# Optimization experiments

Hardware: AMD Instinct MI355X
Metric: run time of the kernel (lower is better)

The kernel has to match this reference:

```python
import jax, jax.numpy as jnp
import numpy as np

N = 50000      # nodes
E = 800000     # edges (avg degree 16)
IN, HID, OUT = 96, 96, 32


def _glorot(key, fan_in, fan_out):
    s = jnp.sqrt(2.0 / (fan_in + fan_out)).astype(jnp.float32)
    return jax.random.normal(key, (fan_in, fan_out), dtype=jnp.float32) * s


def setup_inputs() -> dict:
    key = jax.random.key(0)
    k = jax.random.split(key, 6)
    x = jax.random.normal(k[0], (N, IN), dtype=jnp.float32)
    edge_index = jax.random.randint(k[1], (2, E), 0, N)
    W1 = _glorot(k[2], IN, HID)
    b1 = jnp.zeros((HID,), dtype=jnp.float32)
    W2 = _glorot(k[3], HID, OUT)
    b2 = jnp.zeros((OUT,), dtype=jnp.float32)
    return {"x": x, "edge_index": edge_index, "W1": W1, "b1": b1, "W2": W2, "b2": b2}


def _add_self_loops(edge_index, n):
    loop = jnp.arange(n, dtype=edge_index.dtype)
    src = jnp.concatenate([edge_index[0], loop])
    dst = jnp.concatenate([edge_index[1], loop])
    return src, dst


def _gcn_conv(x, src, dst, W, b, n):
    # PyG GCNConv: linear transform, symmetric deg^-1/2 normalization, scatter-add, bias.
    h = x @ W                                            # [N, F_out]
    ones = jnp.ones(src.shape[0], dtype=x.dtype)
    deg = jax.ops.segment_sum(ones, dst, num_segments=n)  # in-degree incl. self loop
    dinv = jnp.where(deg > 0, jax.lax.rsqrt(deg), 0.0)
    norm = dinv[src] * dinv[dst]                         # [E+N]
    msg = h[src] * norm[:, None]                         # gather + scale
    out = jax.ops.segment_sum(msg, dst, num_segments=n)  # scatter-add
    return out + b


def reference(x, edge_index, W1, b1, W2, b2):
    n = x.shape[0]
    src, dst = _add_self_loops(edge_index, n)
    x1 = jax.nn.relu(_gcn_conv(x, src, dst, W1, b1, n))
    # dropout(p=0.5) is identity in eval mode
    out = _gcn_conv(x1, src, dst, W2, b2, n)
    return (x1, out)
```

## Files before the change

kernel.cpp:

```cpp
#include <hip/hip_runtime.h>


#define NBINS_CAP 256
#define MAXBLK 512
#define CHUNK 2048
#define EBUF 6144
#define WT_LD 104

typedef short short8 __attribute__((ext_vector_type(8)));
typedef float f32x4 __attribute__((ext_vector_type(4)));

__device__ __forceinline__ unsigned short f2bf(float f) {
    unsigned u = __float_as_uint(f);
    u = u + 0x7FFFu + ((u >> 16) & 1u);
    return (unsigned short)(u >> 16);
}
__device__ __forceinline__ float bflo(unsigned w) { return __uint_as_float(w << 16); }
__device__ __forceinline__ float bfhi(unsigned w) { return __uint_as_float(w & 0xFFFF0000u); }

template <int NT>
__global__ __launch_bounds__(NT) void binA_kernel(const int* __restrict__ src,
                                                  const int* __restrict__ dst,
                                                  unsigned* __restrict__ slab,
                                                  int* __restrict__ cntT,
                                                  int* __restrict__ segT,
                                                  int nbins, int E) {
    constexpr int PT = CHUNK / NT;
    __shared__ unsigned ebuf[CHUNK];
    __shared__ int hist[NBINS_CAP];
    __shared__ int cur[NBINS_CAP];
    __shared__ int sc[NT];
    const int tid = threadIdx.x;
    const int beg = blockIdx.x * CHUNK;
    const int cntE = min(CHUNK, E - beg);
    for (int i = tid; i < nbins; i += NT) hist[i] = 0;
    __syncthreads();
    unsigned pv[PT];
    int pb[PT];
#pragma unroll
    for (int j = 0; j < PT; ++j) {
        int idx = j * NT + tid;
        if (idx < cntE) {
            int e = beg + idx;
            int s = src[e], d = dst[e];
            pb[j] = d >> 8;
            pv[j] = ((unsigned)(d & 255) << 16) | (unsigned)s;
            atomicAdd(&hist[pb[j]], 1);
        } else {
            pb[j] = -1;
        }
    }
    __syncthreads();
    int v = (tid < nbins) ? hist[tid] : 0;
    sc[tid] = v;
    __syncthreads();
    for (int off = 1; off < NT; off <<= 1) {
        int t = (tid >= off) ? sc[tid - off] : 0;
        __syncthreads();
        sc[tid] += t;
        __syncthreads();
    }
    if (tid < nbins) cur[tid] = sc[tid] - v;
    __syncthreads();
#pragma unroll
    for (int j = 0; j < PT; ++j) {
        if (pb[j] >= 0) {
            int pos = atomicAdd(&cur[pb[j]], 1);
            ebuf[pos] = pv[j];
        }
    }
    __syncthreads();
    for (int i = tid; i < cntE; i += NT) slab[beg + i] = ebuf[i];
    for (int i = tid; i < nbins; i += NT) {
        cntT[i * MAXBLK + blockIdx.x] = hist[i];
        segT[i * MAXBLK + blockIdx.x] = cur[i] - hist[i];
    }
}

__global__ __launch_bounds__(256) void binsum_kernel(const int* __restrict__ cntT,
                                                     int* __restrict__ btotal,
                                                     const float* __restrict__ W1,
                                                     const float* __restrict__ W2,
                                                     unsigned short* __restrict__ wtg,
                                                     unsigned short* __restrict__ wtg2,
                                                     int nbins, int nblk) {
    __shared__ int r[256];
    const int bin = blockIdx.x, tid = threadIdx.x;
    int s = 0;
    for (int b = tid; b < nblk; b += 256) s += cntT[bin * MAXBLK + b];
    r[tid] = s;
    __syncthreads();
    for (int off = 128; off; off >>= 1) {
        if (tid < off) r[tid] += r[tid + off];
        __syncthreads();
    }
    if (tid == 0) btotal[bin] = r[0];
    const int total = 96 * 96 + 96 * 32;
    const int per = (total + nbins - 1) / nbins;
    for (int j = tid; j < per; j += 256) {
        int idx = bin * per + j;
        if (idx < 96 * 96) {
            int k = idx / 96, f = idx % 96;
            wtg[f * WT_LD + k] = f2bf(W1[idx]);
        } else if (idx < total) {
            int i2 = idx - 96 * 96;
            int k = i2 / 32, f = i2 % 32;
            wtg2[f * WT_LD + k] = f2bf(W2[i2]);
        }
    }
}

__global__ __launch_bounds__(512) void binB_kernel(const unsigned* __restrict__ slab,
                                                   const int* __restrict__ cntT,
                                                   const int* __restrict__ segT,
                                                   const int* __restrict__ btotal,
                                                   float* __restrict__ dinv,
                                                   int* __restrict__ row_ptr,
                                                   unsigned short* __restrict__ esrc,
                                                   int n, int nbins, int nblk, int E) {
    constexpr int NT = 512;
    __shared__ int segc[MAXBLK], pref[MAXBLK], sgs[MAXBLK];
    __shared__ unsigned ebuf[EBUF];
    __shared__ int sc[NT];
    __shared__ int bsc[256];
    __shared__ int hist[256], lbase[256], cur[256];
    const int tid = threadIdx.x;
    const int bin = blockIdx.x;

    if (tid < 256) bsc[tid] = (tid < nbins) ? btotal[tid] : 0;
    __syncthreads();
    for (int off = 1; off < 256; off <<= 1) {
        int t = 0;
        if (tid < 256 && tid >= off) t = bsc[tid - off];
        __syncthreads();
        if (tid < 256) bsc[tid] += t;
        __syncthreads();
    }
    const int base = (bin > 0) ? bsc[bin - 1] : 0;
    if (bin == nbins - 1 && tid == 0) row_ptr[n] = E;
    __syncthreads();

    for (int b = tid; b < MAXBLK; b += NT) {
        segc[b] = (b < nblk) ? cntT[bin * MAXBLK + b] : 0;
        sgs[b]  = (b < nblk) ? segT[bin * MAXBLK + b] : 0;
    }
    if (tid < 256) hist[tid] = 0;
    __syncthreads();
    int v = segc[tid];
    sc[tid] = v;
    __syncthreads();
    for (int off = 1; off < NT; off <<= 1) {
        int t = (tid >= off) ? sc[tid - off] : 0;
        __syncthreads();
        sc[tid] += t;
        __syncthreads();
    }
    pref[tid] = sc[tid] - v;
    __syncthreads();
    const int total = sc[NT - 1];
    const bool fits = (total <= EBUF);

    if (fits) {
        if (tid < nblk) {
            int c = segc[tid];
            const unsigned* p = slab + (size_t)tid * CHUNK + sgs[tid];
            int o = pref[tid];
            for (int i = 0; i < c; ++i) ebuf[o + i] = p[i];
        }
        __syncthreads();
        for (int i = tid; i < total; i += NT) atomicAdd(&hist[ebuf[i] >> 16], 1);
    } else {
        for (int b = tid; b < nblk; b += NT) {
            int c = segc[b];
            const unsigned* p = slab + (size_t)b * CHUNK + sgs[b];
            for (int i = 0; i < c; ++i) atomicAdd(&hist[p[i] >> 16], 1);
        }
    }
    __syncthreads();
    int hv = 0;
    if (tid < 256) { hv = hist[tid]; bsc[tid] = hv; }
    __syncthreads();
    for (int off = 1; off < 256; off <<= 1) {
        int t = 0;
        if (tid < 256 && tid >= off) t = bsc[tid - off];
        __syncthreads();
        if (tid < 256) bsc[tid] += t;
        __syncthreads();
    }
    if (tid < 256) {
        lbase[tid] = bsc[tid] - hv;
        cur[tid] = 0;
        const int node = bin * 256 + tid;
        if (node < n) {
            dinv[node] = rsqrtf((float)hv + 1.0f);
            row_ptr[node] = base + lbase[tid];
        }
    }
    __syncthreads();
    if (fits) {
        for (int i = tid; i < total; i += NT) {
            unsigned e = ebuf[i];
            int local = e >> 16;
            int pos = base + lbase[local] + atomicAdd(&cur[local], 1);
            esrc[pos] = (unsigned short)(e & 0xFFFFu);
        }
    } else {
        for (int b = tid; b < nblk; b += NT) {
            int c = segc[b];
            const unsigned* p = slab + (size_t)b * CHUNK + sgs[b];
            for (int i = 0; i < c; ++i) {
                unsigned e = p[i];
                int local = e >> 16;
                int pos = base + lbase[local] + atomicAdd(&cur[local], 1);
                esrc[pos] = (unsigned short)(e & 0xFFFFu);
            }
        }
    }
}

__global__ __launch_bounds__(256) void gemm1_mfma(const float* __restrict__ X,
                                                  const unsigned short* __restrict__ Wtg,
                                                  const float* __restrict__ dinv,
                                                  unsigned short* __restrict__ Hb, int n) {
    __shared__ unsigned short sWt[96 * WT_LD];
    const int tid = threadIdx.x;
    {
        const uint4* g = (const uint4*)Wtg;
        uint4* s = (uint4*)sWt;
        for (int i = tid; i < 96 * WT_LD * 2 / 16; i += 256) s[i] = g[i];
    }
    __syncthreads();
    const int wave = tid >> 6, lane = tid & 63;
    const int rl = lane & 15, kg = lane >> 4;
    const int row = blockIdx.x * 64 + wave * 16 + rl;
    const int rowc = min(row, n - 1);
    const float* xp = X + (size_t)rowc * 96 + kg * 8;

    f32x4 acc[6];
#pragma unroll
    for (int t = 0; t < 6; ++t) acc[t] = {0.0f, 0.0f, 0.0f, 0.0f};

#pragma unroll
    for (int ks = 0; ks < 3; ++ks) {
        float4 u0 = ((const float4*)(xp + ks * 32))[0];
        float4 u1 = ((const float4*)(xp + ks * 32))[1];
        short8 bfrag;
        bfrag[0] = (short)f2bf(u0.x); bfrag[1] = (short)f2bf(u0.y);
        bfrag[2] = (short)f2bf(u0.z); bfrag[3] = (short)f2bf(u0.w);
        bfrag[4] = (short)f2bf(u1.x); bfrag[5] = (short)f2bf(u1.y);
        bfrag[6] = (short)f2bf(u1.z); bfrag[7] = (short)f2bf(u1.w);
#pragma unroll
        for (int t = 0; t < 6; ++t) {
            short8 afrag = *(const short8*)&sWt[(t * 16 + rl) * WT_LD + ks * 32 + kg * 8];
            acc[t] = __builtin_amdgcn_mfma_f32_16x16x32_bf16(afrag, bfrag, acc[t], 0, 0, 0);
        }
    }
    if (row < n) {
        const float di = dinv[row];
        unsigned short* op = Hb + (size_t)row * 96;
#pragma unroll
        for (int t = 0; t < 6; ++t) {
            unsigned w0 = (unsigned)f2bf(acc[t][0] * di) | ((unsigned)f2bf(acc[t][1] * di) << 16);
            unsigned w1 = (unsigned)f2bf(acc[t][2] * di) | ((unsigned)f2bf(acc[t][3] * di) << 16);
            uint2 w = {w0, w1};
            *(uint2*)(op + t * 16 + kg * 4) = w;
        }
    }
}

__global__ __launch_bounds__(256) void gemm2_mfma(const float* __restrict__ X,
                                                  const unsigned short* __restrict__ Wtg2,
                                                  const float* __restrict__ dinv,
                                                  unsigned short* __restrict__ Hb, int n) {
    __shared__ unsigned short sWt[32 * WT_LD];
    const int tid = threadIdx.x;
    {
        const uint4* g = (const uint4*)Wtg2;
        uint4* s = (uint4*)sWt;
        for (int i = tid; i < 32 * WT_LD * 2 / 16; i += 256) s[i] = g[i];
    }
    __syncthreads();
    const int wave = tid >> 6, lane = tid & 63;
    const int rl = lane & 15, kg = lane >> 4;
    const int row = blockIdx.x * 64 + wave * 16 + rl;
    const int rowc = min(row, n - 1);
    const float* xp = X + (size_t)rowc * 96 + kg * 8;

    f32x4 acc[2];
#pragma unroll
    for (int t = 0; t < 2; ++t) acc[t] = {0.0f, 0.0f, 0.0f, 0.0f};

#pragma unroll
    for (int ks = 0; ks < 3; ++ks) {
        float4 u0 = ((const float4*)(xp + ks * 32))[0];
        float4 u1 = ((const float4*)(xp + ks * 32))[1];
        short8 bfrag;
        bfrag[0] = (short)f2bf(u0.x); bfrag[1] = (short)f2bf(u0.y);
        bfrag[2] = (short)f2bf(u0.z); bfrag[3] = (short)f2bf(u0.w);
        bfrag[4] = (short)f2bf(u1.x); bfrag[5] = (short)f2bf(u1.y);
        bfrag[6] = (short)f2bf(u1.z); bfrag[7] = (short)f2bf(u1.w);
#pragma unroll
        for (int t = 0; t < 2; ++t) {
            short8 afrag = *(const short8*)&sWt[(t * 16 + rl) * WT_LD + ks * 32 + kg * 8];
            acc[t] = __builtin_amdgcn_mfma_f32_16x16x32_bf16(afrag, bfrag, acc[t], 0, 0, 0);
        }
    }
    if (row < n) {
        const float di = dinv[row];
        unsigned short* op = Hb + (size_t)row * 32;
#pragma unroll
        for (int t = 0; t < 2; ++t) {
            unsigned w0 = (unsigned)f2bf(acc[t][0] * di) | ((unsigned)f2bf(acc[t][1] * di) << 16);
            unsigned w1 = (unsigned)f2bf(acc[t][2] * di) | ((unsigned)f2bf(acc[t][3] * di) << 16);
            uint2 w = {w0, w1};
            *(uint2*)(op + t * 16 + kg * 4) = w;
        }
    }
}

#define ACC8(vv)                                                        \
    do {                                                                \
        acc0 += bflo(vv.x); acc1 += bfhi(vv.x);                         \
        acc2 += bflo(vv.y); acc3 += bfhi(vv.y);                         \
        acc4 += bflo(vv.z); acc5 += bfhi(vv.z);                         \
        acc6 += bflo(vv.w); acc7 += bfhi(vv.w);                         \
    } while (0)

template <int FC, int NPB, bool RELU, int NT>
__global__ __launch_bounds__(NT) void agg_kernel(const uint4* __restrict__ H,
                                                 const int* __restrict__ row_ptr,
                                                 const unsigned short* __restrict__ esrc,
                                                 const float* __restrict__ dinv,
                                                 const float* __restrict__ b,
                                                 float* __restrict__ out, int n) {
    constexpr int F = FC * 8;
    const int tid = threadIdx.x;
    const int node = blockIdx.x * NPB + tid / FC;
    const int q = tid % FC;
    if (node >= n) return;
    float acc0 = 0, acc1 = 0, acc2 = 0, acc3 = 0, acc4 = 0, acc5 = 0, acc6 = 0, acc7 = 0;
    {
        uint4 v = H[(size_t)node * FC + q];
        ACC8(v);
    }
    const int beg = row_ptr[node], end = row_ptr[node + 1];
    int e = beg;
    for (; e + 8 <= end; e += 8) {
        int s0 = esrc[e + 0], s1 = esrc[e + 1], s2 = esrc[e + 2], s3 = esrc[e + 3];
        int s4 = esrc[e + 4], s5 = esrc[e + 5], s6 = esrc[e + 6], s7 = esrc[e + 7];
        uint4 v0 = H[(size_t)s0 * FC + q];
        uint4 v1 = H[(size_t)s1 * FC + q];
        uint4 v2 = H[(size_t)s2 * FC + q];
        uint4 v3 = H[(size_t)s3 * FC + q];
        uint4 v4 = H[(size_t)s4 * FC + q];
        uint4 v5 = H[(size_t)s5 * FC + q];
        uint4 v6 = H[(size_t)s6 * FC + q];
        uint4 v7 = H[(size_t)s7 * FC + q];
        ACC8(v0); ACC8(v1); ACC8(v2); ACC8(v3);
        ACC8(v4); ACC8(v5); ACC8(v6); ACC8(v7);
    }
    for (; e + 4 <= end; e += 4) {
        int s0 = esrc[e + 0], s1 = esrc[e + 1], s2 = esrc[e + 2], s3 = esrc[e + 3];
        uint4 v0 = H[(size_t)s0 * FC + q];
        uint4 v1 = H[(size_t)s1 * FC + q];
        uint4 v2 = H[(size_t)s2 * FC + q];
        uint4 v3 = H[(size_t)s3 * FC + q];
        ACC8(v0); ACC8(v1); ACC8(v2); ACC8(v3);
    }
    for (; e < end; ++e) {
        uint4 v = H[(size_t)esrc[e] * FC + q];
        ACC8(v);
    }
    const float di = dinv[node];
    const int f0 = q * 8;
    float4 o0, o1;
    o0.x = acc0 * di + b[f0 + 0];
    o0.y = acc1 * di + b[f0 + 1];
    o0.z = acc2 * di + b[f0 + 2];
    o0.w = acc3 * di + b[f0 + 3];
    o1.x = acc4 * di + b[f0 + 4];
    o1.y = acc5 * di + b[f0 + 5];
    o1.z = acc6 * di + b[f0 + 6];
    o1.w = acc7 * di + b[f0 + 7];
    if (RELU) {
        o0.x = fmaxf(o0.x, 0.0f); o0.y = fmaxf(o0.y, 0.0f);
        o0.z = fmaxf(o0.z, 0.0f); o0.w = fmaxf(o0.w, 0.0f);
        o1.x = fmaxf(o1.x, 0.0f); o1.y = fmaxf(o1.y, 0.0f);
        o1.z = fmaxf(o1.z, 0.0f); o1.w = fmaxf(o1.w, 0.0f);
    }
    float4* op = (float4*)(out + (size_t)node * F);
    op[q * 2 + 0] = o0;
    op[q * 2 + 1] = o1;
}

extern "C" void kernel_launch(void* const* d_in, const int* in_sizes, int n_in,
                              void* d_out, int out_size, void* d_ws, size_t ws_size,
                              hipStream_t stream) {
    const float* x   = (const float*)d_in[0];
    const int*  eidx = (const int*)d_in[1];
    const float* W1  = (const float*)d_in[2];
    const float* b1  = (const float*)d_in[3];
    const float* W2  = (const float*)d_in[4];
    const float* b2  = (const float*)d_in[5];

    const int IN = 96, HID = 96, OUT = 32;
    const int N = in_sizes[0] / IN;
    const int E = in_sizes[1] / 2;
    const int* src = eidx;
    const int* dst = eidx + E;

    float* out  = (float*)d_out;
    float* x1   = out;
    float* out2 = out + (size_t)N * HID;

    const int nbins = (N + 255) / 256;
    const int nblk = (E + CHUNK - 1) / CHUNK;

    auto align512 = [](size_t v) { return ((v + 511) / 512) * 512; };
    char* ws = (char*)d_ws;
    size_t off = 0;
    float* dinv     = (float*)(ws + off); off += align512((size_t)N * 4);
    int* row_ptr    = (int*)(ws + off);   off += align512((size_t)(N + 1) * 4);
    unsigned short* esrc = (unsigned short*)(ws + off); off += align512((size_t)E * 2);
    unsigned* slab  = (unsigned*)(ws + off); off += align512((size_t)E * 4);
    int* cntT       = (int*)(ws + off);   off += align512((size_t)NBINS_CAP * MAXBLK * 4);
    int* segT       = (int*)(ws + off);   off += align512((size_t)NBINS_CAP * MAXBLK * 4);
    int* btotal     = (int*)(ws + off);   off += align512(NBINS_CAP * 4);
    unsigned short* wtg  = (unsigned short*)(ws + off); off += align512(96 * WT_LD * 2);
    unsigned short* wtg2 = (unsigned short*)(ws + off); off += align512(32 * WT_LD * 2);
    unsigned short* hb   = (unsigned short*)(ws + off); off += align512((size_t)N * 96 * 2);

    binA_kernel<256><<<nblk, 256, 0, stream>>>(src, dst, slab, cntT, segT, nbins, E);
    binsum_kernel<<<nbins, 256, 0, stream>>>(cntT, btotal, W1, W2, wtg, wtg2, nbins, nblk);
    binB_kernel<<<nbins, 512, 0, stream>>>(slab, cntT, segT, btotal,
                                           dinv, row_ptr, esrc, N, nbins, nblk, E);

    gemm1_mfma<<<(N + 63) / 64, 256, 0, stream>>>(x, wtg, dinv, hb, N);
    agg_kernel<12, 16, true, 192><<<(N + 15) / 16, 192, 0, stream>>>(
        (const uint4*)hb, row_ptr, esrc, dinv, b1, x1, N);

    gemm2_mfma<<<(N + 63) / 64, 256, 0, stream>>>(x1, wtg2, dinv, hb, N);
    agg_kernel<4, 64, false, 256><<<(N + 63) / 64, 256, 0, stream>>>(
        (const uint4*)hb, row_ptr, esrc, dinv, b2, out2, N);
}
```

Before: 82.66 us.

## Fuse layer-2 GEMM into layer-1 aggregation and drop binsum kernel

The second-layer linear transform is now computed inside the first aggregation kernel from the x1 tile held in shared memory, using scalar FP32 FMAs against W2 staged in LDS. This removes the separate gemm2 launch and the re-read of x1 from global memory. The binsum kernel is removed: per-bin totals are accumulated with global atomics in binA after a memset, and the W1 bf16 conversion moves into binB. The trade-off is a scalar 96x32 matmul per 16-node block (no MFMA), about 14KB of extra LDS per block that may lower occupancy, and global atomic contention on btotal.

```diff
diff --git a/kernel.cpp b/kernel.cpp
--- a/kernel.cpp
+++ b/kernel.cpp
@@ -24,6 +24,7 @@
                                                   unsigned* __restrict__ slab,
                                                   int* __restrict__ cntT,
                                                   int* __restrict__ segT,
+                                                  int* __restrict__ btotal,
                                                   int nbins, int E) {
     constexpr int PT = CHUNK / NT;
     __shared__ unsigned ebuf[CHUNK];
@@ -52,6 +53,7 @@
     }
     __syncthreads();
     int v = (tid < nbins) ? hist[tid] : 0;
+    if (tid < nbins && v) atomicAdd(&btotal[tid], v);
     sc[tid] = v;
     __syncthreads();
     for (int off = 1; off < NT; off <<= 1) {
@@ -77,43 +79,12 @@
     }
 }
 
-__global__ __launch_bounds__(256) void binsum_kernel(const int* __restrict__ cntT,
-                                                     int* __restrict__ btotal,
-                                                     const float* __restrict__ W1,
-                                                     const float* __restrict__ W2,
-                                                     unsigned short* __restrict__ wtg,
-                                                     unsigned short* __restrict__ wtg2,
-                                                     int nbins, int nblk) {
-    __shared__ int r[256];
-    const int bin = blockIdx.x, tid = threadIdx.x;
-    int s = 0;
-    for (int b = tid; b < nblk; b += 256) s += cntT[bin * MAXBLK + b];
-    r[tid] = s;
-    __syncthreads();
-    for (int off = 128; off; off >>= 1) {
-        if (tid < off) r[tid] += r[tid + off];
-        __syncthreads();
-    }
-    if (tid == 0) btotal[bin] = r[0];
-    const int total = 96 * 96 + 96 * 32;
-    const int per = (total + nbins - 1) / nbins;
-    for (int j = tid; j < per; j += 256) {
-        int idx = bin * per + j;
-        if (idx < 96 * 96) {
-            int k = idx / 96, f = idx % 96;
-            wtg[f * WT_LD + k] = f2bf(W1[idx]);
-        } else if (idx < total) {
-            int i2 = idx - 96 * 96;
-            int k = i2 / 32, f = i2 % 32;
-            wtg2[f * WT_LD + k] = f2bf(W2[i2]);
-        }
-    }
-}
-
 __global__ __launch_bounds__(512) void binB_kernel(const unsigned* __restrict__ slab,
                                                    const int* __restrict__ cntT,
                                                    const int* __restrict__ segT,
                                                    const int* __restrict__ btotal,
+                                                   const float* __restrict__ W1,
+                                                   unsigned short* __restrict__ wtg,
                                                    float* __restrict__ dinv,
                                                    int* __restrict__ row_ptr,
                                                    unsigned short* __restrict__ esrc,
@@ -127,6 +98,17 @@
     const int tid = threadIdx.x;
     const int bin = blockIdx.x;
 
+    {
+        const int per = (96 * 96 + gridDim.x - 1) / gridDim.x;
+        for (int j = tid; j < per; j += NT) {
+            int idx = bin * per + j;
+            if (idx < 96 * 96) {
+                int k = idx / 96, f = idx % 96;
+                wtg[f * WT_LD + k] = f2bf(W1[idx]);
+            }
+        }
+    }
+
     if (tid < 256) bsc[tid] = (tid < nbins) ? btotal[tid] : 0;
     __syncthreads();
     for (int off = 1; off < 256; off <<= 1) {
@@ -268,56 +250,6 @@
     }
 }
 
-__global__ __launch_bounds__(256) void gemm2_mfma(const float* __restrict__ X,
-                                                  const unsigned short* __restrict__ Wtg2,
-                                                  const float* __restrict__ dinv,
-                                                  unsigned short* __restrict__ Hb, int n) {
-    __shared__ unsigned short sWt[32 * WT_LD];
-    const int tid = threadIdx.x;
-    {
-        const uint4* g = (const uint4*)Wtg2;
-        uint4* s = (uint4*)sWt;
-        for (int i = tid; i < 32 * WT_LD * 2 / 16; i += 256) s[i] = g[i];
-    }
-    __syncthreads();
-    const int wave = tid >> 6, lane = tid & 63;
-    const int rl = lane & 15, kg = lane >> 4;
-    const int row = blockIdx.x * 64 + wave * 16 + rl;
-    const int rowc = min(row, n - 1);
-    const float* xp = X + (size_t)rowc * 96 + kg * 8;
-
-    f32x4 acc[2];
-#pragma unroll
-    for (int t = 0; t < 2; ++t) acc[t] = {0.0f, 0.0f, 0.0f, 0.0f};
-
-#pragma unroll
-    for (int ks = 0; ks < 3; ++ks) {
-        float4 u0 = ((const float4*)(xp + ks * 32))[0];
-        float4 u1 = ((const float4*)(xp + ks * 32))[1];
-        short8 bfrag;
-        bfrag[0] = (short)f2bf(u0.x); bfrag[1] = (short)f2bf(u0.y);
-        bfrag[2] = (short)f2bf(u0.z); bfrag[3] = (short)f2bf(u0.w);
-        bfrag[4] = (short)f2bf(u1.x); bfrag[5] = (short)f2bf(u1.y);
-        bfrag[6] = (short)f2bf(u1.z); bfrag[7] = (short)f2bf(u1.w);
-#pragma unroll
-        for (int t = 0; t < 2; ++t) {
-            short8 afrag = *(const short8*)&sWt[(t * 16 + rl) * WT_LD + ks * 32 + kg * 8];
-            acc[t] = __builtin_amdgcn_mfma_f32_16x16x32_bf16(afrag, bfrag, acc[t], 0, 0, 0);
-        }
-    }
-    if (row < n) {
-        const float di = dinv[row];
-        unsigned short* op = Hb + (size_t)row * 32;
-#pragma unroll
-        for (int t = 0; t < 2; ++t) {
-            unsigned w0 = (unsigned)f2bf(acc[t][0] * di) | ((unsigned)f2bf(acc[t][1] * di) << 16);
-            unsigned w1 = (unsigned)f2bf(acc[t][2] * di) | ((unsigned)f2bf(acc[t][3] * di) << 16);
-            uint2 w = {w0, w1};
-            *(uint2*)(op + t * 16 + kg * 4) = w;
-        }
-    }
-}
-
 #define ACC8(vv)                                                        \
     do {                                                                \
         acc0 += bflo(vv.x); acc1 += bfhi(vv.x);                         \
@@ -325,6 +257,94 @@
         acc4 += bflo(vv.z); acc5 += bfhi(vv.z);                         \
         acc6 += bflo(vv.w); acc7 += bfhi(vv.w);                         \
     } while (0)
+
+__global__ __launch_bounds__(192) void agg1_fused(const uint4* __restrict__ H,
+                                                  const int* __restrict__ row_ptr,
+                                                  const unsigned short* __restrict__ esrc,
+                                                  const float* __restrict__ dinv,
+                                                  const float* __restrict__ b1,
+                                                  const float* __restrict__ W2,
+                                                  float* __restrict__ x1,
+                                                  unsigned short* __restrict__ hb2, int n) {
+    constexpr int FC = 12, NPB = 16, NT = 192;
+    __shared__ float sx1[NPB][96];
+    __shared__ float sW2[96 * 32];
+    __shared__ float sdi[NPB];
+    const int tid = threadIdx.x;
+    {
+        const float4* g = (const float4*)W2;
+        float4* s = (float4*)sW2;
+        for (int i = tid; i < 96 * 32 / 4; i += NT) s[i] = g[i];
+    }
+    const int nl = tid / FC;
+    const int node = blockIdx.x * NPB + nl;
+    const int q = tid % FC;
+    const bool active = (node < n);
+
+    float acc0 = 0, acc1 = 0, acc2 = 0, acc3 = 0, acc4 = 0, acc5 = 0, acc6 = 0, acc7 = 0;
+    float di = 0.0f;
+    if (active) {
+        {
+            uint4 v = H[(size_t)node * FC + q];
+            ACC8(v);
+        }
+        const int beg = row_ptr[node], end = row_ptr[node + 1];
+        int e = beg;
+        for (; e + 8 <= end; e += 8) {
+            int s0 = esrc[e + 0], s1 = esrc[e + 1], s2 = esrc[e + 2], s3 = esrc[e + 3];
+            int s4 = esrc[e + 4], s5 = esrc[e + 5], s6 = esrc[e + 6], s7 = esrc[e + 7];
+            uint4 v0 = H[(size_t)s0 * FC + q];
+            uint4 v1 = H[(size_t)s1 * FC + q];
+            uint4 v2 = H[(size_t)s2 * FC + q];
+            uint4 v3 = H[(size_t)s3 * FC + q];
+            uint4 v4 = H[(size_t)s4 * FC + q];
+            uint4 v5 = H[(size_t)s5 * FC + q];
+            uint4 v6 = H[(size_t)s6 * FC + q];
+            uint4 v7 = H[(size_t)s7 * FC + q];
+            ACC8(v0); ACC8(v1); ACC8(v2); ACC8(v3);
+            ACC8(v4); ACC8(v5); ACC8(v6); ACC8(v7);
+        }
+        for (; e + 4 <= end; e += 4) {
+            int s0 = esrc[e + 0], s1 = esrc[e + 1], s2 = esrc[e + 2], s3 = esrc[e + 3];
+            uint4 v0 = H[(size_t)s0 * FC + q];
+            uint4 v1 = H[(size_t)s1 * FC + q];
+            uint4 v2 = H[(size_t)s2 * FC + q];
+            uint4 v3 = H[(size_t)s3 * FC + q];
+            ACC8(v0); ACC8(v1); ACC8(v2); ACC8(v3);
+        }
+        for (; e < end; ++e) {
+            uint4 v = H[(size_t)esrc[e] * FC + q];
+            ACC8(v);
+        }
+        di = dinv[node];
+        if (q == 0) sdi[nl] = di;
+        const int f0 = q * 8;
+        float4 o0, o1;
+        o0.x = fmaxf(acc0 * di + b1[f0 + 0], 0.0f);
+        o0.y = fmaxf(acc1 * di + b1[f0 + 1], 0.0f);
+        o0.z = fmaxf(acc2 * di + b1[f0 + 2], 0.0f);
+        o0.w = fmaxf(acc3 * di + b1[f0 + 3], 0.0f);
+        o1.x = fmaxf(acc4 * di + b1[f0 + 4], 0.0f);
+        o1.y = fmaxf(acc5 * di + b1[f0 + 5], 0.0f);
+        o1.z = fmaxf(acc6 * di + b1[f0 + 6], 0.0f);
+        o1.w = fmaxf(acc7 * di + b1[f0 + 7], 0.0f);
+        float4* op = (float4*)(x1 + (size_t)node * 96);
+        op[q * 2 + 0] = o0;
+        op[q * 2 + 1] = o1;
+        *(float4*)&sx1[nl][f0] = o0;
+        *(float4*)&sx1[nl][f0 + 4] = o1;
+    }
+    __syncthreads();
+    for (int j = tid; j < NPB * 32; j += NT) {
+        const int nl2 = j >> 5, o = j & 31;
+        const int row2 = blockIdx.x * NPB + nl2;
+        if (row2 >= n) continue;
+        float a = 0.0f;
+#pragma unroll 8
+        for (int k = 0; k < 96; ++k) a += sx1[nl2][k] * sW2[k * 32 + o];
+        hb2[(size_t)row2 * 32 + o] = f2bf(a * sdi[nl2]);
+    }
+}
 
 template <int FC, int NPB, bool RELU, int NT>
 __global__ __launch_bounds__(NT) void agg_kernel(const uint4* __restrict__ H,
@@ -426,20 +446,19 @@
     int* cntT       = (int*)(ws + off);   off += align512((size_t)NBINS_CAP * MAXBLK * 4);
     int* segT       = (int*)(ws + off);   off += align512((size_t)NBINS_CAP * MAXBLK * 4);
     int* btotal     = (int*)(ws + off);   off += align512(NBINS_CAP * 4);
-    unsigned short* wtg  = (unsigned short*)(ws + off); off += align512(96 * WT_LD * 2);
-    unsigned short* wtg2 = (unsigned short*)(ws + off); off += align512(32 * WT_LD * 2);
-    unsigned short* hb   = (unsigned short*)(ws + off); off += align512((size_t)N * 96 * 2);
-
-    binA_kernel<256><<<nblk, 256, 0, stream>>>(src, dst, slab, cntT, segT, nbins, E);
-    binsum_kernel<<<nbins, 256, 0, stream>>>(cntT, btotal, W1, W2, wtg, wtg2, nbins, nblk);
-    binB_kernel<<<nbins, 512, 0, stream>>>(slab, cntT, segT, btotal,
+    unsigned short* wtg = (unsigned short*)(ws + off); off += align512(96 * WT_LD * 2);
+    unsigned short* hb  = (unsigned short*)(ws + off); off += align512((size_t)N * 96 * 2);
+    unsigned short* hb2 = (unsigned short*)(ws + off); off += align512((size_t)N * 32 * 2);
+
+    hipMemsetAsync(btotal, 0, NBINS_CAP * sizeof(int), stream);
+    binA_kernel<256><<<nblk, 256, 0, stream>>>(src, dst, slab, cntT, segT, btotal, nbins, E);
+    binB_kernel<<<nbins, 512, 0, stream>>>(slab, cntT, segT, btotal, W1, wtg,
                                            dinv, row_ptr, esrc, N, nbins, nblk, E);
 
     gemm1_mfma<<<(N + 63) / 64, 256, 0, stream>>>(x, wtg, dinv, hb, N);
-    agg_kernel<12, 16, true, 192><<<(N + 15) / 16, 192, 0, stream>>>(
-        (const uint4*)hb, row_ptr, esrc, dinv, b1, x1, N);
-
-    gemm2_mfma<<<(N + 63) / 64, 256, 0, stream>>>(x1, wtg2, dinv, hb, N);
+    agg1_fused<<<(N + 15) / 16, 192, 0, stream>>>(
+        (const uint4*)hb, row_ptr, esrc, dinv, b1, W2, x1, hb2, N);
+
     agg_kernel<4, 64, false, 256><<<(N + 63) / 64, 256, 0, stream>>>(
-        (const uint4*)hb, row_ptr, esrc, dinv, b2, out2, N);
-}
+        (const uint4*)hb2, row_ptr, esrc, dinv, b2, out2, N);
+}
```

New measurement: 94.54 us. 14.4% more time.
